# Optimization experiments

Measured on AMD Instinct MI355X. Metric: run time of the kernel, lower is better.

## Reference

```python
import jax, jax.numpy as jnp
import numpy as np

B, C, H, W = 8, 512, 32, 32
NUM_HEADS = 8


def setup_inputs() -> dict:
    key = jax.random.key(0)
    ks = jax.random.split(key, 7)
    s = 0.02
    return {
        "x": jax.random.normal(ks[0], (B, C, H, W), dtype=jnp.float32),
        "Wq": jax.random.normal(ks[1], (C, C), dtype=jnp.float32) * s,
        "bq": jax.random.normal(ks[2], (C,), dtype=jnp.float32) * s,
        "Wk": jax.random.normal(ks[3], (C, C), dtype=jnp.float32) * s,
        "bk": jax.random.normal(ks[4], (C,), dtype=jnp.float32) * s,
        "Wv": jax.random.normal(ks[5], (C, C), dtype=jnp.float32) * s,
        "bv": jax.random.normal(ks[6], (C,), dtype=jnp.float32) * s,
        "gamma": jnp.zeros((1,), dtype=jnp.float32),
    }


def reference(x, Wq, bq, Wk, bk, Wv, bv, gamma):
    b, c, h, w = x.shape
    nh = NUM_HEADS
    hd = c // nh
    n = h * w

    def proj(Wt, bt):
        # 1x1 conv == per-pixel linear: [b,c,h,w] x [o,c] -> [b,o,h,w]
        return jnp.einsum('bchw,oc->bohw', x, Wt) + bt[None, :, None, None]

    q = proj(Wq, bq).reshape(b, nh, hd, n).transpose(0, 1, 3, 2)  # [b,nh,n,hd]
    k = proj(Wk, bk).reshape(b, nh, hd, n)                         # [b,nh,hd,n]
    v = proj(Wv, bv).reshape(b, nh, hd, n).transpose(0, 1, 3, 2)   # [b,nh,n,hd]

    energy = jnp.einsum('bhnd,bhdm->bhnm', q, k)  # NOTE: no 1/sqrt(d) scale (faithful)
    attention = jax.nn.softmax(energy, axis=-1)
    out = jnp.einsum('bhnm,bhmd->bhnd', attention, v)  # [b,nh,n,hd]
    out = out.transpose(0, 1, 3, 2).reshape(b, c, h, w)
    return gamma * out + x
```

## Files before the change

kernel.cpp:

```cpp
#include <hip/hip_runtime.h>
#include <cstdint>
#include <cstddef>

typedef float floatx4 __attribute__((ext_vector_type(4)));
typedef short shortx2 __attribute__((ext_vector_type(2)));
typedef short shortx4 __attribute__((ext_vector_type(4)));
typedef short shortx8 __attribute__((ext_vector_type(8)));
typedef int   intx2  __attribute__((ext_vector_type(2)));

#define LDS_AS __attribute__((address_space(3)))
#define GLB_AS __attribute__((address_space(1)))

#define MFMA_16x16x32_BF16(A, B, C) __builtin_amdgcn_mfma_f32_16x16x32_bf16(A, B, C, 0, 0, 0)

#if defined(__HIP_DEVICE_COMPILE__)
  #if __has_builtin(__builtin_amdgcn_mfma_f32_16x16x16bf16_1k)
    #define MFMA_16x16x16_BF16(A, B, C) __builtin_amdgcn_mfma_f32_16x16x16bf16_1k(A, B, C, 0, 0, 0)
  #else
    #error "gfx950 device pass lacks __builtin_amdgcn_mfma_f32_16x16x16bf16_1k"
  #endif
#else
  #define MFMA_16x16x16_BF16(A, B, C) (C)
#endif

#define LOG2E 1.44269504088896340736f

__device__ __forceinline__ unsigned short f2bf(float f) {
    unsigned int u = __float_as_uint(f);
    u += 0x7fffu + ((u >> 16) & 1u);
    return (unsigned short)(u >> 16);
}

__device__ __forceinline__ float exp2f_fast(float x) {
#if defined(__HIP_DEVICE_COMPILE__) && __has_builtin(__builtin_amdgcn_exp2f)
    return __builtin_amdgcn_exp2f(x);
#else
    return exp2f(x);
#endif
}

__device__ __forceinline__ shortx4 pk4(float a, float b, float c, float d) {
#if defined(__HIP_DEVICE_COMPILE__) && __has_builtin(__builtin_amdgcn_cvt_pk_bf16_f32)
    typedef __bf16 bf16x2_t __attribute__((ext_vector_type(2)));
    bf16x2_t lo = __builtin_amdgcn_cvt_pk_bf16_f32(a, b);
    bf16x2_t hi = __builtin_amdgcn_cvt_pk_bf16_f32(c, d);
    intx2 p; p[0] = __builtin_bit_cast(int, lo); p[1] = __builtin_bit_cast(int, hi);
    return __builtin_bit_cast(shortx4, p);
#else
    unsigned int ua = __float_as_uint(a), ub = __float_as_uint(b);
    unsigned int uc = __float_as_uint(c), ud = __float_as_uint(d);
    intx2 p;
    p[0] = (int)((ua >> 16) | (ub & 0xffff0000u));
    p[1] = (int)((uc >> 16) | (ud & 0xffff0000u));
    return __builtin_bit_cast(shortx4, p);
#endif
}

__device__ __forceinline__ void gll16(const void* g, void* l) {
    __builtin_amdgcn_global_load_lds((const GLB_AS uint32_t*)g, (LDS_AS uint32_t*)l, 16, 0, 0);
}


__global__ __launch_bounds__(256) void prep_kernel(
    const float* __restrict__ x,
    const float* __restrict__ Wq, const float* __restrict__ Wk, const float* __restrict__ Wv,
    unsigned short* __restrict__ xT, unsigned short* __restrict__ Wb)
{
    const int bid = blockIdx.x;
    const int t = threadIdx.x;
    if (bid < 1024) {
        __shared__ alignas(16) unsigned short sT[64][72];
        const int b = bid >> 7, rem = bid & 127;
        const int c0 = (rem >> 4) * 64, p0 = (rem & 15) * 64;
        const int cl = (t >> 4) * 4, p4 = (t & 15) * 4;
        float4 v[4];
#pragma unroll
        for (int di = 0; di < 4; ++di)
            v[di] = *(const float4*)(x + (size_t)(b * 512 + c0 + cl + di) * 1024 + p0 + p4);
#pragma unroll
        for (int j = 0; j < 4; ++j) {
            shortx4 pk;
#pragma unroll
            for (int dd = 0; dd < 4; ++dd)
                pk[dd] = (short)f2bf(((const float*)&v[dd])[j]);
            *(shortx4*)&sT[p4 + j][cl] = pk;
        }
        __syncthreads();
        const int p = t >> 2, ch = (t & 3) * 16;
        const size_t base = ((size_t)b * 1024 + p0 + p) * 512 + c0 + ch;
        *(shortx8*)&xT[base] = *(const shortx8*)&sT[p][ch];
        *(shortx8*)&xT[base + 8] = *(const shortx8*)&sT[p][ch + 8];
    } else {
        const int wb = bid - 1024;
        const int mat = wb >> 6;
        const float* src = (mat == 0) ? Wq : (mat == 1) ? Wk : Wv;
        const int off0 = (wb & 63) * 4096;
#pragma unroll
        for (int r = 0; r < 4; ++r) {
            const int idx = off0 + r * 1024 + t * 4;
            const float4 v = *(const float4*)(src + idx);
            shortx4 pk;
            pk[0] = (short)f2bf(v.x); pk[1] = (short)f2bf(v.y);
            pk[2] = (short)f2bf(v.z); pk[3] = (short)f2bf(v.w);
            *(shortx4*)&Wb[(size_t)mat * 262144 + idx] = pk;
        }
    }
}

__global__ __launch_bounds__(256, 4) void proj_kernel(
    const unsigned short* __restrict__ Wb, const unsigned short* __restrict__ xT,
    const float* __restrict__ bq, const float* __restrict__ bk, const float* __restrict__ bv,
    unsigned short* __restrict__ Qg, unsigned short* __restrict__ Kg,
    unsigned short* __restrict__ Vg)
{
    __shared__ union {
        struct { unsigned short W[2][3][32][32]; unsigned short X[2][128][32]; } s;
        unsigned short Ep[128][40];
    } u;

    const int tid = threadIdx.x;
    const int w = tid >> 6, lane = tid & 63;
    const int quad = lane >> 4, l16 = lane & 15;
    const int id = blockIdx.x;
    const int oo = id & 1;
    const int p0 = ((id >> 1) & 7) * 128;
    const int bh = id >> 4, b = bh >> 3, h = bh & 7;
    const int o0 = h * 64 + oo * 32;

    floatx4 acc[3][2][2];
#pragma unroll
    for (int t = 0; t < 3; ++t) {
        const float* bsrc = (t == 0) ? bq : (t == 1) ? bk : bv;
#pragma unroll
        for (int ot = 0; ot < 2; ++ot) {
            floatx4 bi;
#pragma unroll
            for (int i = 0; i < 4; ++i)
                bi[i] = bsrc[o0 + ot * 16 + quad * 4 + i];
#pragma unroll
            for (int pt = 0; pt < 2; ++pt) acc[t][ot][pt] = bi;
        }
    }

    auto stage = [&](int ks, int bfi) {
        const int c0 = ks * 32;
#pragma unroll
        for (int jj = 0; jj < 4; ++jj) {
            const int j = jj * 4 + w;
            if (j < 6) {
                const int rf0 = j * 16;
                const int rf = rf0 + (lane >> 2);
                const int mt = rf >> 5, r = rf & 31;
                const int cl = (lane & 3) ^ (r & 3);
                gll16(Wb + (size_t)mt * 262144 + (size_t)(o0 + r) * 512 + c0 + cl * 8,
                      &u.s.W[bfi][0][0][0] + rf0 * 32);
            } else if (j < 14) {
                const int r0 = (j - 6) * 16;
                const int r = r0 + (lane >> 2);
                const int cl = (lane & 3) ^ (r & 3);
                gll16(xT + (size_t)(b * 1024 + p0 + r) * 512 + c0 + cl * 8,
                      &u.s.X[bfi][0][0] + r0 * 32);
            }
        }
    };

    stage(0, 0);
    for (int ks = 0; ks < 16; ++ks) {
        __syncthreads();
        if (ks + 1 < 16) stage(ks + 1, (ks + 1) & 1);
        const int bfi = ks & 1;
        shortx8 af[3][2], bx[2];
#pragma unroll
        for (int t = 0; t < 3; ++t)
#pragma unroll
            for (int ot = 0; ot < 2; ++ot) {
                const int r = ot * 16 + l16;
                const int pc = quad ^ (r & 3);
                af[t][ot] = *(const shortx8*)&u.s.W[bfi][t][r][pc * 8];
            }
#pragma unroll
        for (int pt = 0; pt < 2; ++pt) {
            const int r = w * 32 + pt * 16 + l16;
            const int pc = quad ^ (r & 3);
            bx[pt] = *(const shortx8*)&u.s.X[bfi][r][pc * 8];
        }
#pragma unroll
        for (int t = 0; t < 3; ++t)
#pragma unroll
            for (int ot = 0; ot < 2; ++ot)
#pragma unroll
                for (int pt = 0; pt < 2; ++pt)
                    acc[t][ot][pt] = MFMA_16x16x32_BF16(af[t][ot], bx[pt], acc[t][ot][pt]);
    }

#pragma unroll
    for (int ot = 0; ot < 2; ++ot)
#pragma unroll
        for (int pt = 0; pt < 2; ++pt)
#pragma unroll
            for (int i = 0; i < 4; ++i) {
                const int d = oo * 32 + ot * 16 + quad * 4 + i;
                const int p = p0 + w * 32 + pt * 16 + l16;
                Vg[((size_t)bh * 64 + d) * 1024 + p] = f2bf(acc[2][ot][pt][i]);
            }
#pragma unroll
    for (int t = 0; t < 2; ++t) {
        const float scale = (t == 0) ? LOG2E : 1.0f;
        __syncthreads();
#pragma unroll
        for (int ot = 0; ot < 2; ++ot)
#pragma unroll
            for (int pt = 0; pt < 2; ++pt)
#pragma unroll
                for (int i = 0; i < 4; ++i)
                    u.Ep[w * 32 + pt * 16 + l16][ot * 16 + quad * 4 + i] =
                        f2bf(acc[t][ot][pt][i] * scale);
        __syncthreads();
        unsigned short* G = (t == 0) ? Qg : Kg;
        const int p = tid >> 1, ch = (tid & 1) * 16;
        const size_t base = ((size_t)bh * 1024 + p0 + p) * 64 + oo * 32 + ch;
        *(shortx8*)&G[base]     = *(const shortx8*)&u.Ep[p][ch];
        *(shortx8*)&G[base + 8] = *(const shortx8*)&u.Ep[p][ch + 8];
    }
}

__global__ __launch_bounds__(256, 2) void attn_kernel(
    const unsigned short* __restrict__ Qg, const unsigned short* __restrict__ Kg,
    const unsigned short* __restrict__ Vg, const float* __restrict__ x,
    const float* __restrict__ gamma, float* __restrict__ out)
{
    __shared__ alignas(16) unsigned short sK[2][64][64];
    __shared__ alignas(16) unsigned short sV[2][64][64];

    const int tid = threadIdx.x;
    const int w = tid >> 6, lane = tid & 63;
    const int quad = lane >> 4, l16 = lane & 15;
    const int bh = blockIdx.x, b = bh >> 3, h = bh & 7;
    const int p0 = blockIdx.y * 128;
    const int pw = p0 + w * 32;

    shortx8 aq[2][2];
#pragma unroll
    for (int pt = 0; pt < 2; ++pt)
#pragma unroll
        for (int ks = 0; ks < 2; ++ks)
            aq[pt][ks] = *(const shortx8*)
                &Qg[((size_t)bh * 1024 + pw + pt * 16 + l16) * 64 + ks * 32 + quad * 8];

    floatx4 oacc[2][4];
#pragma unroll
    for (int pt = 0; pt < 2; ++pt)
#pragma unroll
        for (int dt = 0; dt < 4; ++dt) oacc[pt][dt] = (floatx4)0.0f;
    floatx4 lacc[2] = {(floatx4)0.0f, (floatx4)0.0f};
    const shortx4 ones4 = {(short)0x3F80, (short)0x3F80, (short)0x3F80, (short)0x3F80};

    auto stage = [&](int kt, int bfi) {
        const int m0 = kt * 64;
#pragma unroll
        for (int kv = 0; kv < 2; ++kv) {
            const int r0 = w * 16 + kv * 8;
            const int r = r0 + (lane >> 3);
            const int cl = (lane & 7) ^ (r & 7);
            gll16(Kg + ((size_t)bh * 1024 + m0 + r) * 64 + cl * 8, &sK[bfi][0][0] + r0 * 64);
            gll16(Vg + ((size_t)bh * 64 + r) * 1024 + m0 + cl * 8, &sV[bfi][0][0] + r0 * 64);
        }
    };

    stage(0, 0);
    for (int kt = 0; kt < 16; ++kt) {
        __syncthreads();
        if (kt + 1 < 16) stage(kt + 1, (kt + 1) & 1);
        const int bfi = kt & 1;

        floatx4 s[2][4];
#pragma unroll
        for (int pt = 0; pt < 2; ++pt)
#pragma unroll
            for (int nt = 0; nt < 4; ++nt) s[pt][nt] = (floatx4)0.0f;
#pragma unroll
        for (int nt = 0; nt < 4; ++nt)
#pragma unroll
            for (int ks = 0; ks < 2; ++ks) {
                const int r = nt * 16 + l16;
                const int pc = (ks * 4 + quad) ^ (r & 7);
                const shortx8 ak = *(const shortx8*)&sK[bfi][r][pc * 8];
#pragma unroll
                for (int pt = 0; pt < 2; ++pt)
                    s[pt][nt] = MFMA_16x16x32_BF16(ak, aq[pt][ks], s[pt][nt]);
            }

        shortx4 bp[2][4];
#pragma unroll
        for (int pt = 0; pt < 2; ++pt)
#pragma unroll
            for (int mt = 0; mt < 4; ++mt) {
                float e0 = exp2f_fast(s[pt][mt][0]);
                float e1 = exp2f_fast(s[pt][mt][1]);
                float e2 = exp2f_fast(s[pt][mt][2]);
                float e3 = exp2f_fast(s[pt][mt][3]);
                bp[pt][mt] = pk4(e0, e1, e2, e3);
            }

#pragma unroll
        for (int dt = 0; dt < 4; ++dt)
#pragma unroll
            for (int mt = 0; mt < 4; ++mt) {
                const int r = dt * 16 + l16;
                const int pc = (mt * 2 + (quad >> 1)) ^ (r & 7);
                const shortx4 av = *(const shortx4*)&sV[bfi][r][pc * 8 + (quad & 1) * 4];
#pragma unroll
                for (int pt = 0; pt < 2; ++pt)
                    oacc[pt][dt] = MFMA_16x16x16_BF16(av, bp[pt][mt], oacc[pt][dt]);
            }
#pragma unroll
        for (int mt = 0; mt < 4; ++mt)
#pragma unroll
            for (int pt = 0; pt < 2; ++pt)
                lacc[pt] = MFMA_16x16x16_BF16(ones4, bp[pt][mt], lacc[pt]);
    }

    const float g = gamma[0];
    const float invl[2] = {1.0f / lacc[0][0], 1.0f / lacc[1][0]};
#pragma unroll
    for (int pt = 0; pt < 2; ++pt)
#pragma unroll
        for (int dt = 0; dt < 4; ++dt)
#pragma unroll
            for (int i = 0; i < 4; ++i) {
                const int d = dt * 16 + quad * 4 + i;
                const int p = pw + pt * 16 + l16;
                const size_t idx = ((size_t)b * 512 + h * 64 + d) * 1024 + p;
                out[idx] = g * (oacc[pt][dt][i] * invl[pt]) + x[idx];
            }
}

extern "C" void kernel_launch(void* const* d_in, const int* in_sizes, int n_in,
                              void* d_out, int out_size, void* d_ws, size_t ws_size,
                              hipStream_t stream) {
    const float* x     = (const float*)d_in[0];
    const float* Wq    = (const float*)d_in[1];
    const float* bq    = (const float*)d_in[2];
    const float* Wk    = (const float*)d_in[3];
    const float* bk    = (const float*)d_in[4];
    const float* Wv    = (const float*)d_in[5];
    const float* bv    = (const float*)d_in[6];
    const float* gamma = (const float*)d_in[7];
    float* out = (float*)d_out;

    unsigned short* xT = (unsigned short*)d_ws;
    unsigned short* Wb = xT + 4194304;
    unsigned short* Qg = Wb + 786432;
    unsigned short* Kg = Qg + 4194304;
    unsigned short* Vg = Kg + 4194304;

    prep_kernel<<<1216, 256, 0, stream>>>(x, Wq, Wk, Wv, xT, Wb);
    proj_kernel<<<1024, 256, 0, stream>>>(Wb, xT, bq, bk, bv, Qg, Kg, Vg);
    attn_kernel<<<dim3(64, 8), 256, 0, stream>>>(Qg, Kg, Vg, x, gamma, out);
}
```

Before: 132.3 us.

## Replace LDS staging with direct global-to-register loads in proj and attention kernels

Both the projection and attention kernels drop their double-buffered LDS staging through global_load_lds and the per-iteration __syncthreads. Each wave now loads its MFMA operands straight from global memory into registers, relying on L2/L1 cache for reuse across waves. The attention kernel software-prefetches the next K tile into registers. This removes barrier and LDS traffic but makes every wave re-fetch shared tiles from cache, raises register pressure, and uses less coalesced loads, especially the short V loads.

```diff
diff --git a/kernel.cpp b/kernel.cpp
--- a/kernel.cpp
+++ b/kernel.cpp
@@ -3,13 +3,9 @@
 #include <cstddef>
 
 typedef float floatx4 __attribute__((ext_vector_type(4)));
-typedef short shortx2 __attribute__((ext_vector_type(2)));
 typedef short shortx4 __attribute__((ext_vector_type(4)));
 typedef short shortx8 __attribute__((ext_vector_type(8)));
 typedef int   intx2  __attribute__((ext_vector_type(2)));
-
-#define LDS_AS __attribute__((address_space(3)))
-#define GLB_AS __attribute__((address_space(1)))
 
 #define MFMA_16x16x32_BF16(A, B, C) __builtin_amdgcn_mfma_f32_16x16x32_bf16(A, B, C, 0, 0, 0)
 
@@ -56,10 +52,6 @@
 #endif
 }
 
-__device__ __forceinline__ void gll16(const void* g, void* l) {
-    __builtin_amdgcn_global_load_lds((const GLB_AS uint32_t*)g, (LDS_AS uint32_t*)l, 16, 0, 0);
-}
-
 
 __global__ __launch_bounds__(256) void prep_kernel(
     const float* __restrict__ x,
@@ -113,10 +105,7 @@
     unsigned short* __restrict__ Qg, unsigned short* __restrict__ Kg,
     unsigned short* __restrict__ Vg)
 {
-    __shared__ union {
-        struct { unsigned short W[2][3][32][32]; unsigned short X[2][128][32]; } s;
-        unsigned short Ep[128][40];
-    } u;
+    __shared__ alignas(16) unsigned short Ep[128][40];
 
     const int tid = threadIdx.x;
     const int w = tid >> 6, lane = tid & 63;
@@ -142,48 +131,29 @@
         }
     }
 
-    auto stage = [&](int ks, int bfi) {
+    const unsigned short* wrow[3][2];
+#pragma unroll
+    for (int t = 0; t < 3; ++t)
+#pragma unroll
+        for (int ot = 0; ot < 2; ++ot)
+            wrow[t][ot] = Wb + (size_t)t * 262144 + (size_t)(o0 + ot * 16 + l16) * 512 + quad * 8;
+    const unsigned short* xrow[2];
+#pragma unroll
+    for (int pt = 0; pt < 2; ++pt)
+        xrow[pt] = xT + ((size_t)b * 1024 + p0 + w * 32 + pt * 16 + l16) * 512 + quad * 8;
+
+#pragma unroll 2
+    for (int ks = 0; ks < 16; ++ks) {
         const int c0 = ks * 32;
-#pragma unroll
-        for (int jj = 0; jj < 4; ++jj) {
-            const int j = jj * 4 + w;
-            if (j < 6) {
-                const int rf0 = j * 16;
-                const int rf = rf0 + (lane >> 2);
-                const int mt = rf >> 5, r = rf & 31;
-                const int cl = (lane & 3) ^ (r & 3);
-                gll16(Wb + (size_t)mt * 262144 + (size_t)(o0 + r) * 512 + c0 + cl * 8,
-                      &u.s.W[bfi][0][0][0] + rf0 * 32);
-            } else if (j < 14) {
-                const int r0 = (j - 6) * 16;
-                const int r = r0 + (lane >> 2);
-                const int cl = (lane & 3) ^ (r & 3);
-                gll16(xT + (size_t)(b * 1024 + p0 + r) * 512 + c0 + cl * 8,
-                      &u.s.X[bfi][0][0] + r0 * 32);
-            }
-        }
-    };
-
-    stage(0, 0);
-    for (int ks = 0; ks < 16; ++ks) {
-        __syncthreads();
-        if (ks + 1 < 16) stage(ks + 1, (ks + 1) & 1);
-        const int bfi = ks & 1;
         shortx8 af[3][2], bx[2];
 #pragma unroll
         for (int t = 0; t < 3; ++t)
 #pragma unroll
-            for (int ot = 0; ot < 2; ++ot) {
-                const int r = ot * 16 + l16;
-                const int pc = quad ^ (r & 3);
-                af[t][ot] = *(const shortx8*)&u.s.W[bfi][t][r][pc * 8];
-            }
-#pragma unroll
-        for (int pt = 0; pt < 2; ++pt) {
-            const int r = w * 32 + pt * 16 + l16;
-            const int pc = quad ^ (r & 3);
-            bx[pt] = *(const shortx8*)&u.s.X[bfi][r][pc * 8];
-        }
+            for (int ot = 0; ot < 2; ++ot)
+                af[t][ot] = *(const shortx8*)(wrow[t][ot] + c0);
+#pragma unroll
+        for (int pt = 0; pt < 2; ++pt)
+            bx[pt] = *(const shortx8*)(xrow[pt] + c0);
 #pragma unroll
         for (int t = 0; t < 3; ++t)
 #pragma unroll
@@ -213,14 +183,14 @@
             for (int pt = 0; pt < 2; ++pt)
 #pragma unroll
                 for (int i = 0; i < 4; ++i)
-                    u.Ep[w * 32 + pt * 16 + l16][ot * 16 + quad * 4 + i] =
+                    Ep[w * 32 + pt * 16 + l16][ot * 16 + quad * 4 + i] =
                         f2bf(acc[t][ot][pt][i] * scale);
         __syncthreads();
         unsigned short* G = (t == 0) ? Qg : Kg;
         const int p = tid >> 1, ch = (tid & 1) * 16;
         const size_t base = ((size_t)bh * 1024 + p0 + p) * 64 + oo * 32 + ch;
-        *(shortx8*)&G[base]     = *(const shortx8*)&u.Ep[p][ch];
-        *(shortx8*)&G[base + 8] = *(const shortx8*)&u.Ep[p][ch + 8];
+        *(shortx8*)&G[base]     = *(const shortx8*)&Ep[p][ch];
+        *(shortx8*)&G[base + 8] = *(const shortx8*)&Ep[p][ch + 8];
     }
 }
 
@@ -229,15 +199,14 @@
     const unsigned short* __restrict__ Vg, const float* __restrict__ x,
     const float* __restrict__ gamma, float* __restrict__ out)
 {
-    __shared__ alignas(16) unsigned short sK[2][64][64];
-    __shared__ alignas(16) unsigned short sV[2][64][64];
-
     const int tid = threadIdx.x;
     const int w = tid >> 6, lane = tid & 63;
     const int quad = lane >> 4, l16 = lane & 15;
     const int bh = blockIdx.x, b = bh >> 3, h = bh & 7;
-    const int p0 = blockIdx.y * 128;
-    const int pw = p0 + w * 32;
+    const int pw = blockIdx.y * 128 + w * 32;
+
+    const unsigned short* Kb = Kg + (size_t)bh * 65536;
+    const unsigned short* Vb = Vg + (size_t)bh * 65536;
 
     shortx8 aq[2][2];
 #pragma unroll
@@ -255,23 +224,31 @@
     floatx4 lacc[2] = {(floatx4)0.0f, (floatx4)0.0f};
     const shortx4 ones4 = {(short)0x3F80, (short)0x3F80, (short)0x3F80, (short)0x3F80};
 
-    auto stage = [&](int kt, int bfi) {
+    shortx8 akc[4][2], akn[4][2];
+#pragma unroll
+    for (int nt = 0; nt < 4; ++nt)
+#pragma unroll
+        for (int ks = 0; ks < 2; ++ks)
+            akc[nt][ks] = *(const shortx8*)&Kb[(nt * 16 + l16) * 64 + ks * 32 + quad * 8];
+
+    for (int kt = 0; kt < 16; ++kt) {
         const int m0 = kt * 64;
-#pragma unroll
-        for (int kv = 0; kv < 2; ++kv) {
-            const int r0 = w * 16 + kv * 8;
-            const int r = r0 + (lane >> 3);
-            const int cl = (lane & 7) ^ (r & 7);
-            gll16(Kg + ((size_t)bh * 1024 + m0 + r) * 64 + cl * 8, &sK[bfi][0][0] + r0 * 64);
-            gll16(Vg + ((size_t)bh * 64 + r) * 1024 + m0 + cl * 8, &sV[bfi][0][0] + r0 * 64);
+        if (kt + 1 < 16) {
+            const int m1 = m0 + 64;
+#pragma unroll
+            for (int nt = 0; nt < 4; ++nt)
+#pragma unroll
+                for (int ks = 0; ks < 2; ++ks)
+                    akn[nt][ks] = *(const shortx8*)
+                        &Kb[(m1 + nt * 16 + l16) * 64 + ks * 32 + quad * 8];
         }
-    };
-
-    stage(0, 0);
-    for (int kt = 0; kt < 16; ++kt) {
-        __syncthreads();
-        if (kt + 1 < 16) stage(kt + 1, (kt + 1) & 1);
-        const int bfi = kt & 1;
+        shortx4 av[4][4];
+#pragma unroll
+        for (int dt = 0; dt < 4; ++dt)
+#pragma unroll
+            for (int mt = 0; mt < 4; ++mt)
+                av[dt][mt] = *(const shortx4*)
+                    &Vb[(dt * 16 + l16) * 1024 + m0 + mt * 16 + quad * 4];
 
         floatx4 s[2][4];
 #pragma unroll
@@ -281,14 +258,10 @@
 #pragma unroll
         for (int nt = 0; nt < 4; ++nt)
 #pragma unroll
-            for (int ks = 0; ks < 2; ++ks) {
-                const int r = nt * 16 + l16;
-                const int pc = (ks * 4 + quad) ^ (r & 7);
-                const shortx8 ak = *(const shortx8*)&sK[bfi][r][pc * 8];
+            for (int ks = 0; ks < 2; ++ks)
 #pragma unroll
                 for (int pt = 0; pt < 2; ++pt)
-                    s[pt][nt] = MFMA_16x16x32_BF16(ak, aq[pt][ks], s[pt][nt]);
-            }
+                    s[pt][nt] = MFMA_16x16x32_BF16(akc[nt][ks], aq[pt][ks], s[pt][nt]);
 
         shortx4 bp[2][4];
 #pragma unroll
@@ -305,19 +278,21 @@
 #pragma unroll
         for (int dt = 0; dt < 4; ++dt)
 #pragma unroll
-            for (int mt = 0; mt < 4; ++mt) {
-                const int r = dt * 16 + l16;
-                const int pc = (mt * 2 + (quad >> 1)) ^ (r & 7);
-                const shortx4 av = *(const shortx4*)&sV[bfi][r][pc * 8 + (quad & 1) * 4];
+            for (int mt = 0; mt < 4; ++mt)
 #pragma unroll
                 for (int pt = 0; pt < 2; ++pt)
-                    oacc[pt][dt] = MFMA_16x16x16_BF16(av, bp[pt][mt], oacc[pt][dt]);
-            }
+                    oacc[pt][dt] = MFMA_16x16x16_BF16(av[dt][mt], bp[pt][mt], oacc[pt][dt]);
 #pragma unroll
         for (int mt = 0; mt < 4; ++mt)
 #pragma unroll
             for (int pt = 0; pt < 2; ++pt)
                 lacc[pt] = MFMA_16x16x16_BF16(ones4, bp[pt][mt], lacc[pt]);
+
+#pragma unroll
+        for (int nt = 0; nt < 4; ++nt)
+#pragma unroll
+            for (int ks = 0; ks < 2; ++ks)
+                akc[nt][ks] = akn[nt][ks];
     }
 
     const float g = gamma[0];
```

Measured after the change: 235.6 us. 1.78x slower.

## Halve attention query tile per block to double grid and occupancy

Applied to the files above, without the earlier changes.

Each wave now handles 16 query rows instead of 32, so a block covers 64 queries and the grid doubles to 64x16 blocks. Launch bounds are raised to allow 4 blocks per CU, and register use per thread drops. In exchange, K/V tiles staged into LDS are reused by half as many queries, which doubles global K/V traffic and LDS reads per unit of MFMA work.

```diff
diff --git a/kernel.cpp b/kernel.cpp
--- a/kernel.cpp
+++ b/kernel.cpp
@@ -3,7 +3,6 @@
 #include <cstddef>
 
 typedef float floatx4 __attribute__((ext_vector_type(4)));
-typedef short shortx2 __attribute__((ext_vector_type(2)));
 typedef short shortx4 __attribute__((ext_vector_type(4)));
 typedef short shortx8 __attribute__((ext_vector_type(8)));
 typedef int   intx2  __attribute__((ext_vector_type(2)));
@@ -224,7 +223,7 @@
     }
 }
 
-__global__ __launch_bounds__(256, 2) void attn_kernel(
+__global__ __launch_bounds__(256, 4) void attn_kernel(
     const unsigned short* __restrict__ Qg, const unsigned short* __restrict__ Kg,
     const unsigned short* __restrict__ Vg, const float* __restrict__ x,
     const float* __restrict__ gamma, float* __restrict__ out)
@@ -236,23 +235,18 @@
     const int w = tid >> 6, lane = tid & 63;
     const int quad = lane >> 4, l16 = lane & 15;
     const int bh = blockIdx.x, b = bh >> 3, h = bh & 7;
-    const int p0 = blockIdx.y * 128;
-    const int pw = p0 + w * 32;
-
-    shortx8 aq[2][2];
-#pragma unroll
-    for (int pt = 0; pt < 2; ++pt)
-#pragma unroll
-        for (int ks = 0; ks < 2; ++ks)
-            aq[pt][ks] = *(const shortx8*)
-                &Qg[((size_t)bh * 1024 + pw + pt * 16 + l16) * 64 + ks * 32 + quad * 8];
-
-    floatx4 oacc[2][4];
-#pragma unroll
-    for (int pt = 0; pt < 2; ++pt)
-#pragma unroll
-        for (int dt = 0; dt < 4; ++dt) oacc[pt][dt] = (floatx4)0.0f;
-    floatx4 lacc[2] = {(floatx4)0.0f, (floatx4)0.0f};
+    const int pw = blockIdx.y * 64 + w * 16;
+
+    shortx8 aq[2];
+#pragma unroll
+    for (int ks = 0; ks < 2; ++ks)
+        aq[ks] = *(const shortx8*)
+            &Qg[((size_t)bh * 1024 + pw + l16) * 64 + ks * 32 + quad * 8];
+
+    floatx4 oacc[4];
+#pragma unroll
+    for (int dt = 0; dt < 4; ++dt) oacc[dt] = (floatx4)0.0f;
+    floatx4 lacc = (floatx4)0.0f;
     const shortx4 ones4 = {(short)0x3F80, (short)0x3F80, (short)0x3F80, (short)0x3F80};
 
     auto stage = [&](int kt, int bfi) {
@@ -273,11 +267,9 @@
         if (kt + 1 < 16) stage(kt + 1, (kt + 1) & 1);
         const int bfi = kt & 1;
 
-        floatx4 s[2][4];
-#pragma unroll
-        for (int pt = 0; pt < 2; ++pt)
-#pragma unroll
-            for (int nt = 0; nt < 4; ++nt) s[pt][nt] = (floatx4)0.0f;
+        floatx4 s[4];
+#pragma unroll
+        for (int nt = 0; nt < 4; ++nt) s[nt] = (floatx4)0.0f;
 #pragma unroll
         for (int nt = 0; nt < 4; ++nt)
 #pragma unroll
@@ -285,22 +277,18 @@
                 const int r = nt * 16 + l16;
                 const int pc = (ks * 4 + quad) ^ (r & 7);
                 const shortx8 ak = *(const shortx8*)&sK[bfi][r][pc * 8];
-#pragma unroll
-                for (int pt = 0; pt < 2; ++pt)
-                    s[pt][nt] = MFMA_16x16x32_BF16(ak, aq[pt][ks], s[pt][nt]);
-            }
-
-        shortx4 bp[2][4];
-#pragma unroll
-        for (int pt = 0; pt < 2; ++pt)
-#pragma unroll
-            for (int mt = 0; mt < 4; ++mt) {
-                float e0 = exp2f_fast(s[pt][mt][0]);
-                float e1 = exp2f_fast(s[pt][mt][1]);
-                float e2 = exp2f_fast(s[pt][mt][2]);
-                float e3 = exp2f_fast(s[pt][mt][3]);
-                bp[pt][mt] = pk4(e0, e1, e2, e3);
-            }
+                s[nt] = MFMA_16x16x32_BF16(ak, aq[ks], s[nt]);
+            }
+
+        shortx4 bp[4];
+#pragma unroll
+        for (int mt = 0; mt < 4; ++mt) {
+            float e0 = exp2f_fast(s[mt][0]);
+            float e1 = exp2f_fast(s[mt][1]);
+            float e2 = exp2f_fast(s[mt][2]);
+            float e3 = exp2f_fast(s[mt][3]);
+            bp[mt] = pk4(e0, e1, e2, e3);
+        }
 
 #pragma unroll
         for (int dt = 0; dt < 4; ++dt)
@@ -309,30 +297,24 @@
                 const int r = dt * 16 + l16;
                 const int pc = (mt * 2 + (quad >> 1)) ^ (r & 7);
                 const shortx4 av = *(const shortx4*)&sV[bfi][r][pc * 8 + (quad & 1) * 4];
-#pragma unroll
-                for (int pt = 0; pt < 2; ++pt)
-                    oacc[pt][dt] = MFMA_16x16x16_BF16(av, bp[pt][mt], oacc[pt][dt]);
+                oacc[dt] = MFMA_16x16x16_BF16(av, bp[mt], oacc[dt]);
             }
 #pragma unroll
         for (int mt = 0; mt < 4; ++mt)
-#pragma unroll
-            for (int pt = 0; pt < 2; ++pt)
-                lacc[pt] = MFMA_16x16x16_BF16(ones4, bp[pt][mt], lacc[pt]);
+            lacc = MFMA_16x16x16_BF16(ones4, bp[mt], lacc);
     }
 
     const float g = gamma[0];
-    const float invl[2] = {1.0f / lacc[0][0], 1.0f / lacc[1][0]};
-#pragma unroll
-    for (int pt = 0; pt < 2; ++pt)
-#pragma unroll
-        for (int dt = 0; dt < 4; ++dt)
-#pragma unroll
-            for (int i = 0; i < 4; ++i) {
-                const int d = dt * 16 + quad * 4 + i;
-                const int p = pw + pt * 16 + l16;
-                const size_t idx = ((size_t)b * 512 + h * 64 + d) * 1024 + p;
-                out[idx] = g * (oacc[pt][dt][i] * invl[pt]) + x[idx];
-            }
+    const float invl = 1.0f / lacc[0];
+#pragma unroll
+    for (int dt = 0; dt < 4; ++dt)
+#pragma unroll
+        for (int i = 0; i < 4; ++i) {
+            const int d = dt * 16 + quad * 4 + i;
+            const int p = pw + l16;
+            const size_t idx = ((size_t)b * 512 + h * 64 + d) * 1024 + p;
+            out[idx] = g * (oacc[dt][i] * invl) + x[idx];
+        }
 }
 
 extern "C" void kernel_launch(void* const* d_in, const int* in_sizes, int n_in,
@@ -356,5 +338,5 @@
 
     prep_kernel<<<1216, 256, 0, stream>>>(x, Wq, Wk, Wv, xT, Wb);
     proj_kernel<<<1024, 256, 0, stream>>>(Wb, xT, bq, bk, bv, Qg, Kg, Vg);
-    attn_kernel<<<dim3(64, 8), 256, 0, stream>>>(Qg, Kg, Vg, x, gamma, out);
-}
+    attn_kernel<<<dim3(64, 16), 256, 0, stream>>>(Qg, Kg, Vg, x, gamma, out);
+}
```

Result: faster. 128.3 us (-3.0%).

## Switch attention kernel to single-wave blocks with barrier-free single-buffered staging

Applied to the files above, without the earlier changes.

Each attention block now holds one wavefront that processes 32 query rows, so the grid has four times as many blocks. The K and V tiles are single-buffered, and manual waitcnt instructions replace the __syncthreads barriers, letting the QK^T step start once K has arrived while V is still loading. The trade-off is that each block now loads the full K/V tile itself instead of sharing it across four waves, which quadruples global and L2 traffic for K/V. Prefetch of the next tile no longer overlaps with the PV step.

```diff
diff --git a/kernel.cpp b/kernel.cpp
--- a/kernel.cpp
+++ b/kernel.cpp
@@ -3,7 +3,6 @@
 #include <cstddef>
 
 typedef float floatx4 __attribute__((ext_vector_type(4)));
-typedef short shortx2 __attribute__((ext_vector_type(2)));
 typedef short shortx4 __attribute__((ext_vector_type(4)));
 typedef short shortx8 __attribute__((ext_vector_type(8)));
 typedef int   intx2  __attribute__((ext_vector_type(2)));
@@ -224,20 +223,21 @@
     }
 }
 
-__global__ __launch_bounds__(256, 2) void attn_kernel(
+__global__ __launch_bounds__(64, 2) void attn_kernel(
     const unsigned short* __restrict__ Qg, const unsigned short* __restrict__ Kg,
     const unsigned short* __restrict__ Vg, const float* __restrict__ x,
     const float* __restrict__ gamma, float* __restrict__ out)
 {
-    __shared__ alignas(16) unsigned short sK[2][64][64];
-    __shared__ alignas(16) unsigned short sV[2][64][64];
-
-    const int tid = threadIdx.x;
-    const int w = tid >> 6, lane = tid & 63;
+    __shared__ alignas(16) unsigned short sK[64][64];
+    __shared__ alignas(16) unsigned short sV[64][64];
+
+    const int lane = threadIdx.x;
     const int quad = lane >> 4, l16 = lane & 15;
     const int bh = blockIdx.x, b = bh >> 3, h = bh & 7;
-    const int p0 = blockIdx.y * 128;
-    const int pw = p0 + w * 32;
+    const int pw = blockIdx.y * 32;
+
+    const unsigned short* KgB = Kg + (size_t)bh * 65536;
+    const unsigned short* VgB = Vg + (size_t)bh * 65536;
 
     shortx8 aq[2][2];
 #pragma unroll
@@ -255,23 +255,25 @@
     floatx4 lacc[2] = {(floatx4)0.0f, (floatx4)0.0f};
     const shortx4 ones4 = {(short)0x3F80, (short)0x3F80, (short)0x3F80, (short)0x3F80};
 
-    auto stage = [&](int kt, int bfi) {
+    const int rstage = lane >> 3;
+    const int clx    = lane & 7;
+
+    for (int kt = 0; kt < 16; ++kt) {
         const int m0 = kt * 64;
-#pragma unroll
-        for (int kv = 0; kv < 2; ++kv) {
-            const int r0 = w * 16 + kv * 8;
-            const int r = r0 + (lane >> 3);
-            const int cl = (lane & 7) ^ (r & 7);
-            gll16(Kg + ((size_t)bh * 1024 + m0 + r) * 64 + cl * 8, &sK[bfi][0][0] + r0 * 64);
-            gll16(Vg + ((size_t)bh * 64 + r) * 1024 + m0 + cl * 8, &sV[bfi][0][0] + r0 * 64);
-        }
-    };
-
-    stage(0, 0);
-    for (int kt = 0; kt < 16; ++kt) {
-        __syncthreads();
-        if (kt + 1 < 16) stage(kt + 1, (kt + 1) & 1);
-        const int bfi = kt & 1;
+        asm volatile("s_waitcnt lgkmcnt(0)" ::: "memory");
+#pragma unroll
+        for (int ii = 0; ii < 8; ++ii) {
+            const int r = ii * 8 + rstage;
+            const int cl = clx ^ (r & 7);
+            gll16(KgB + (size_t)(m0 + r) * 64 + cl * 8, &sK[0][0] + ii * 512);
+        }
+#pragma unroll
+        for (int ii = 0; ii < 8; ++ii) {
+            const int r = ii * 8 + rstage;
+            const int cl = clx ^ (r & 7);
+            gll16(VgB + (size_t)r * 1024 + m0 + cl * 8, &sV[0][0] + ii * 512);
+        }
+        asm volatile("s_waitcnt vmcnt(8)" ::: "memory");
 
         floatx4 s[2][4];
 #pragma unroll
@@ -284,7 +286,7 @@
             for (int ks = 0; ks < 2; ++ks) {
                 const int r = nt * 16 + l16;
                 const int pc = (ks * 4 + quad) ^ (r & 7);
-                const shortx8 ak = *(const shortx8*)&sK[bfi][r][pc * 8];
+                const shortx8 ak = *(const shortx8*)&sK[r][pc * 8];
 #pragma unroll
                 for (int pt = 0; pt < 2; ++pt)
                     s[pt][nt] = MFMA_16x16x32_BF16(ak, aq[pt][ks], s[pt][nt]);
@@ -302,13 +304,15 @@
                 bp[pt][mt] = pk4(e0, e1, e2, e3);
             }
 
+        asm volatile("s_waitcnt vmcnt(0)" ::: "memory");
+
 #pragma unroll
         for (int dt = 0; dt < 4; ++dt)
 #pragma unroll
             for (int mt = 0; mt < 4; ++mt) {
                 const int r = dt * 16 + l16;
                 const int pc = (mt * 2 + (quad >> 1)) ^ (r & 7);
-                const shortx4 av = *(const shortx4*)&sV[bfi][r][pc * 8 + (quad & 1) * 4];
+                const shortx4 av = *(const shortx4*)&sV[r][pc * 8 + (quad & 1) * 4];
 #pragma unroll
                 for (int pt = 0; pt < 2; ++pt)
                     oacc[pt][dt] = MFMA_16x16x16_BF16(av, bp[pt][mt], oacc[pt][dt]);
@@ -356,5 +360,5 @@
 
     prep_kernel<<<1216, 256, 0, stream>>>(x, Wq, Wk, Wv, xT, Wb);
     proj_kernel<<<1024, 256, 0, stream>>>(Wb, xT, bq, bk, bv, Qg, Kg, Vg);
-    attn_kernel<<<dim3(64, 8), 256, 0, stream>>>(Qg, Kg, Vg, x, gamma, out);
-}
+    attn_kernel<<<dim3(64, 32), 64, 0, stream>>>(Qg, Kg, Vg, x, gamma, out);
+}
```

New measurement: 132.1 us. About the same (-0.2%).
